# Performance work log

Measured on AMD Instinct MI355X. Metric: run time of the kernel, lower is better.

The kernel has to match this reference:

```python
import jax, jax.numpy as jnp
import numpy as np

B, NB, DIM = 4096, 64, 256
CNT_R = 500
CNT_E = CNT_R * 2  # padding relation id == CNT_E maps to the masked row
N_WR = CNT_R * 2 + 1
N_ZQ = CNT_R * 2


def setup_inputs() -> dict:
    key = jax.random.key(0)
    ks = jax.random.split(key, 10)
    batch_nei_rid = jax.random.randint(ks[0], (B, NB), 0, N_WR, dtype=jnp.int64 if jax.config.read('jax_enable_x64') else jnp.int32)
    batch_nei_e_emb = jax.random.normal(ks[1], (B, NB, DIM), dtype=jnp.float32)
    batch_nei_rw = jax.random.uniform(ks[2], (B, NB), dtype=jnp.float32)
    batch_q_rid = jax.random.randint(ks[3], (B,), 0, N_ZQ, dtype=jnp.int32)
    # xavier-normal-ish params
    def xav(k, shape):
        fan_in, fan_out = shape[-1], shape[-2] if len(shape) > 1 else shape[-1]
        std = (2.0 / (fan_in + fan_out)) ** 0.5
        return (jax.random.normal(k, shape) * std).astype(jnp.float32)
    w_r_weight = xav(ks[4], (N_WR, DIM))
    zq_weight = xav(ks[5], (N_ZQ, DIM))
    attn_W_w = xav(ks[6], (2 * DIM, 2 * DIM))   # [out, in], torch Linear layout
    attn_W_b = jnp.zeros((2 * DIM,), jnp.float32)
    u_a_w = xav(ks[7], (1, 2 * DIM))
    u_a_b = jnp.zeros((1,), jnp.float32)
    return {
        'batch_nei_rid': batch_nei_rid,
        'batch_nei_e_emb': batch_nei_e_emb,
        'batch_nei_rw': batch_nei_rw,
        'batch_q_rid': batch_q_rid,
        'w_r_weight': w_r_weight,
        'zq_weight': zq_weight,
        'attn_W_w': attn_W_w,
        'attn_W_b': attn_W_b,
        'u_a_w': u_a_w,
        'u_a_b': u_a_b,
    }


def reference(batch_nei_rid, batch_nei_e_emb, batch_nei_rw, batch_q_rid,
              w_r_weight, zq_weight, attn_W_w, attn_W_b, u_a_w, u_a_b):
    # relation hyperplane gather + TransH-style projection
    w_r = w_r_weight[batch_nei_rid]                                   # [B,NB,D]
    nrm = jnp.maximum(jnp.linalg.norm(w_r, axis=-1, keepdims=True), 1e-12)
    wn = w_r / nrm                                                    # f.normalize(p=2)
    e_tr = batch_nei_e_emb - jnp.sum(batch_nei_e_emb * wn, axis=-1, keepdims=True) * wn
    # mask_emb: 1 for real rows, 0 for padding row (index CNT_E)
    mask = (batch_nei_rid < CNT_E).astype(e_tr.dtype)[..., None]
    e_tr = e_tr * mask
    # nn attention: concat(z_q, e_Tr) -> Linear -> tanh -> Linear(1)
    z_q = zq_weight[batch_q_rid][:, None, :]                          # [B,1,D]
    cat = jnp.concatenate([jnp.broadcast_to(z_q, e_tr.shape), e_tr], axis=-1)  # [B,NB,2D]
    h = jnp.tanh(jnp.einsum('bni,oi->bno', cat, attn_W_w) + attn_W_b)
    _alpha = jnp.einsum('bni,oi->bno', h, u_a_w)[..., 0] + u_a_b[0]   # [B,NB]
    # mask_weight: 1e19 at padding row, subtracted before softmax
    _alpha = _alpha - jnp.where(batch_nei_rid == CNT_E, jnp.asarray(1e19, _alpha.dtype), jnp.asarray(0.0, _alpha.dtype))
    alpha = jax.nn.softmax(_alpha, axis=-1)
    attn = alpha + batch_nei_rw                                       # use_logic_attention
    return jnp.sum(attn[..., None] * e_tr, axis=-2)                   # [B,D]
```

## Files before the change

### kernel.cpp

```cpp
#include <hip/hip_runtime.h>
#include <math.h>

#define NB    64
#define DIM   256
#define TWOD  512
#define CNTE  1000
#define E2S   264

typedef __attribute__((ext_vector_type(8))) short short8;
typedef __attribute__((ext_vector_type(4))) float f32x4;

union U16x8 { uint4 u; short8 s; };

__device__ __forceinline__ unsigned short f2bf(float x) {
    unsigned int u = __float_as_uint(x);
    u += 0x7fffu + ((u >> 16) & 1u);
    return (unsigned short)(u >> 16);
}
__device__ __forceinline__ float bf2f(unsigned short h) {
    return __uint_as_float(((unsigned int)h) << 16);
}
__device__ __forceinline__ float tanh_fast(float x) {
    float e = __expf(2.0f * x);
    return 1.0f - 2.0f / (e + 1.0f);
}

__global__ __launch_bounds__(256) void pack_w_kernel(
    const float* __restrict__ attn_W, unsigned short* __restrict__ wbf)
{
    int f = blockIdx.x * 256 + threadIdx.x;
    int j    = f & 7;
    int lane = (f >> 3) & 63;
    int kt   = (f >> 9) & 15;
    int ot   = f >> 13;
    int o = ot * 16 + (lane & 15);
    int k = kt * 32 + (lane >> 4) * 8 + j;
    wbf[f] = f2bf(attn_W[(size_t)o * TWOD + k]);
}

__global__ __launch_bounds__(256, 2) void encoder_attn_kernel(
    const int*   __restrict__ nei_rid,
    const float* __restrict__ nei_e,
    const float* __restrict__ nei_rw,
    const int*   __restrict__ q_rid,
    const float* __restrict__ w_r,
    const float* __restrict__ zq_w,
    const float* __restrict__ attn_b,
    const float* __restrict__ u_a_w,
    const float* __restrict__ u_a_b,
    const unsigned short* __restrict__ wbf,
    float*       __restrict__ out)
{
    __shared__ __align__(16) unsigned short e2[NB * E2S];
    __shared__ __align__(16) unsigned short zq2[DIM];
    __shared__ float2 bua[TWOD];
    __shared__ float  red_a[256];
    __shared__ float  pen[NB];
    __shared__ float  attn_lds[NB];

    const int b = blockIdx.x;
    const int t = threadIdx.x;

    const int qr = q_rid[b];
    bua[t]       = make_float2(attn_b[t],       u_a_w[t]);
    bua[t + 256] = make_float2(attn_b[t + 256], u_a_w[t + 256]);
    zq2[t] = f2bf(zq_w[(size_t)qr * DIM + t]);

    const int n = t >> 2, q = t & 3;
    const int rid = nei_rid[b * NB + n];
    const float4* e4 = (const float4*)(nei_e + ((size_t)(b * NB + n)) * DIM) + q * 16;
    const float4* w4 = (const float4*)(w_r + (size_t)rid * DIM) + q * 16;
    {
        float4 ev[16], wv[16];
        float sew = 0.f, sww = 0.f;
        #pragma unroll
        for (int j = 0; j < 16; ++j) {
            ev[j] = e4[j]; wv[j] = w4[j];
            sew += ev[j].x * wv[j].x + ev[j].y * wv[j].y + ev[j].z * wv[j].z + ev[j].w * wv[j].w;
            sww += wv[j].x * wv[j].x + wv[j].y * wv[j].y + wv[j].z * wv[j].z + wv[j].w * wv[j].w;
        }
        sew += __shfl_xor(sew, 1); sew += __shfl_xor(sew, 2);
        sww += __shfl_xor(sww, 1); sww += __shfl_xor(sww, 2);
        float nc   = fmaxf(sqrtf(sww), 1e-12f);
        float coef = sew / (nc * nc);
        float maskf = (rid < CNTE) ? 1.f : 0.f;
        if (q == 0) pen[n] = (rid == CNTE) ? 1e19f : 0.f;
        unsigned short* e2row = e2 + n * E2S + q * 64;
        #pragma unroll
        for (int jj = 0; jj < 8; ++jj) {
            float4 e0 = ev[jj * 2],     w0 = wv[jj * 2];
            float4 e1 = ev[jj * 2 + 1], w1 = wv[jj * 2 + 1];
            uint4 pk;
            pk.x = (unsigned int)f2bf((e0.x - coef * w0.x) * maskf)
                 | ((unsigned int)f2bf((e0.y - coef * w0.y) * maskf) << 16);
            pk.y = (unsigned int)f2bf((e0.z - coef * w0.z) * maskf)
                 | ((unsigned int)f2bf((e0.w - coef * w0.w) * maskf) << 16);
            pk.z = (unsigned int)f2bf((e1.x - coef * w1.x) * maskf)
                 | ((unsigned int)f2bf((e1.y - coef * w1.y) * maskf) << 16);
            pk.w = (unsigned int)f2bf((e1.z - coef * w1.z) * maskf)
                 | ((unsigned int)f2bf((e1.w - coef * w1.w) * maskf) << 16);
            *(uint4*)(e2row + jj * 8) = pk;
        }
    }
    __syncthreads();

    const int wv_id = t >> 6;
    const int lane  = t & 63;
    const int l15 = lane & 15, lq = lane >> 4;

    short8 afrag[4][8];
    #pragma unroll
    for (int mt = 0; mt < 4; ++mt)
        #pragma unroll
        for (int kt = 0; kt < 8; ++kt) {
            const unsigned short* p = e2 + (mt * 16 + l15) * E2S + kt * 32 + lq * 8;
            U16x8 u; u.u = *(const uint4*)p;
            afrag[mt][kt] = u.s;
        }

    f32x4 lpv[4];
    #pragma unroll
    for (int mt = 0; mt < 4; ++mt) lpv[mt] = (f32x4){0.f, 0.f, 0.f, 0.f};

    #pragma unroll 1
    for (int ot = 0; ot < 8; ++ot) {
        const int otg = wv_id * 8 + ot;
        const uint4* wp = (const uint4*)wbf + (size_t)(otg * 16) * 64 + lane;
        short8 bz[8], be[8];
        #pragma unroll
        for (int kt = 0; kt < 8; ++kt) { U16x8 u; u.u = wp[kt * 64]; bz[kt] = u.s; }
        #pragma unroll
        for (int kt = 0; kt < 8; ++kt) { U16x8 u; u.u = wp[(kt + 8) * 64]; be[kt] = u.s; }

        f32x4 accz = (f32x4){0.f, 0.f, 0.f, 0.f};
        #pragma unroll
        for (int kt = 0; kt < 8; ++kt) {
            U16x8 u; u.u = *(const uint4*)(zq2 + kt * 32 + lq * 8);
            accz = __builtin_amdgcn_mfma_f32_16x16x32_bf16(u.s, bz[kt], accz, 0, 0, 0);
        }
        f32x4 acc[4];
        #pragma unroll
        for (int mt = 0; mt < 4; ++mt) acc[mt] = accz;
        #pragma unroll
        for (int kt = 0; kt < 8; ++kt)
            #pragma unroll
            for (int mt = 0; mt < 4; ++mt)
                acc[mt] = __builtin_amdgcn_mfma_f32_16x16x32_bf16(
                              afrag[mt][kt], be[kt], acc[mt], 0, 0, 0);

        float2 zu = bua[otg * 16 + l15];
        #pragma unroll
        for (int mt = 0; mt < 4; ++mt)
            #pragma unroll
            for (int r = 0; r < 4; ++r) {
                float h = tanh_fast(acc[mt][r] + zu.x);
                lpv[mt][r] += zu.y * h;
            }
    }

    #pragma unroll
    for (int mt = 0; mt < 4; ++mt)
        #pragma unroll
        for (int r = 0; r < 4; ++r) {
            float v = lpv[mt][r];
            v += __shfl_xor(v, 1); v += __shfl_xor(v, 2);
            v += __shfl_xor(v, 4); v += __shfl_xor(v, 8);
            if (l15 == 0) red_a[wv_id * 64 + mt * 16 + lq * 4 + r] = v;
        }
    __syncthreads();

    if (t < NB) {
        float lgt = red_a[t] + red_a[64 + t] + red_a[128 + t] + red_a[192 + t]
                  + u_a_b[0] - pen[t];
        float m = lgt;
        #pragma unroll
        for (int off = 32; off > 0; off >>= 1) m = fmaxf(m, __shfl_xor(m, off));
        float ex = __expf(lgt - m);
        float s = ex;
        #pragma unroll
        for (int off = 32; off > 0; off >>= 1) s += __shfl_xor(s, off);
        attn_lds[t] = ex / s + nei_rw[b * NB + t];
    }
    __syncthreads();

    float oacc = 0.f;
    #pragma unroll 8
    for (int nn = 0; nn < NB; ++nn)
        oacc += attn_lds[nn] * bf2f(e2[nn * E2S + t]);
    out[(size_t)b * DIM + t] = oacc;
}

extern "C" void kernel_launch(void* const* d_in, const int* in_sizes, int n_in,
                              void* d_out, int out_size, void* d_ws, size_t ws_size,
                              hipStream_t stream) {
    const int*   nei_rid = (const int*)  d_in[0];
    const float* nei_e   = (const float*)d_in[1];
    const float* nei_rw  = (const float*)d_in[2];
    const int*   q_rid   = (const int*)  d_in[3];
    const float* w_r     = (const float*)d_in[4];
    const float* zq_w    = (const float*)d_in[5];
    const float* attn_W  = (const float*)d_in[6];
    const float* attn_b  = (const float*)d_in[7];
    const float* u_a_w   = (const float*)d_in[8];
    const float* u_a_b   = (const float*)d_in[9];
    float* out = (float*)d_out;

    const int B = in_sizes[3];

    unsigned short* wbf = (unsigned short*)d_ws;

    hipLaunchKernelGGL(pack_w_kernel, dim3(1024), dim3(256), 0, stream, attn_W, wbf);
    hipLaunchKernelGGL(encoder_attn_kernel, dim3(B), dim3(256), 0, stream,
                       nei_rid, nei_e, nei_rw, q_rid, w_r, zq_w,
                       attn_b, u_a_w, u_a_b, wbf, out);
}
```

Measured before the change: 526.4 us.

## Precompute z_q projection per query id and restructure MFMA loop over k

Splits the attention linear layer: the z_q half is precomputed once per query relation id (1000 ids) in a separate fp32 kernel and gathered per batch row, so only the e_tr half (K=256) runs as bf16 MFMA. A fallback computes the z_q projection inside the block when workspace is too small. The MFMA loop is reordered to hold all 8 output tiles of accumulators and stream A fragments per k-step, and tanh is folded algebraically into a reciprocal, dropping the constant u_a_b and bias terms that cancel in softmax. The neighbour projection is reworked so 8 threads handle each row over two halves. Holding more accumulators raises register pressure, and the extra launch adds a small fixed cost.

```diff
diff --git a/kernel.cpp b/kernel.cpp
--- a/kernel.cpp
+++ b/kernel.cpp
@@ -6,6 +6,7 @@
 #define TWOD  512
 #define CNTE  1000
 #define E2S   264
+#define NQ    1000
 
 typedef __attribute__((ext_vector_type(8))) short short8;
 typedef __attribute__((ext_vector_type(4))) float f32x4;
@@ -20,9 +21,37 @@
 __device__ __forceinline__ float bf2f(unsigned short h) {
     return __uint_as_float(((unsigned int)h) << 16);
 }
-__device__ __forceinline__ float tanh_fast(float x) {
-    float e = __expf(2.0f * x);
-    return 1.0f - 2.0f / (e + 1.0f);
+
+__global__ __launch_bounds__(256) void zpre_kernel(
+    const float* __restrict__ zq_w, const float* __restrict__ attn_W,
+    const float* __restrict__ attn_b, float* __restrict__ zpre)
+{
+    __shared__ float zq[8][DIM];
+    const int t  = threadIdx.x;
+    const int q0 = blockIdx.x * 8;
+    #pragma unroll
+    for (int r = 0; r < 8; ++r) zq[r][t] = zq_w[(size_t)(q0 + r) * DIM + t];
+    __syncthreads();
+    #pragma unroll
+    for (int half = 0; half < 2; ++half) {
+        const int o = t + half * 256;
+        const float4* wrow = (const float4*)(attn_W + (size_t)o * TWOD);
+        float acc[8];
+        #pragma unroll
+        for (int r = 0; r < 8; ++r) acc[r] = 0.f;
+        #pragma unroll 4
+        for (int kk = 0; kk < 64; ++kk) {
+            float4 w = wrow[kk];
+            #pragma unroll
+            for (int r = 0; r < 8; ++r)
+                acc[r] += w.x * zq[r][kk * 4 + 0] + w.y * zq[r][kk * 4 + 1]
+                        + w.z * zq[r][kk * 4 + 2] + w.w * zq[r][kk * 4 + 3];
+        }
+        const float bo = attn_b[o];
+        #pragma unroll
+        for (int r = 0; r < 8; ++r)
+            zpre[(size_t)(q0 + r) * TWOD + o] = acc[r] + bo;
+    }
 }
 
 __global__ __launch_bounds__(256) void pack_w_kernel(
@@ -31,11 +60,11 @@
     int f = blockIdx.x * 256 + threadIdx.x;
     int j    = f & 7;
     int lane = (f >> 3) & 63;
-    int kt   = (f >> 9) & 15;
-    int ot   = f >> 13;
-    int o = ot * 16 + (lane & 15);
-    int k = kt * 32 + (lane >> 4) * 8 + j;
-    wbf[f] = f2bf(attn_W[(size_t)o * TWOD + k]);
+    int kt   = (f >> 9) & 7;
+    int ot   = f >> 12;
+    int o  = ot * 16 + (lane & 15);
+    int ke = kt * 32 + (lane >> 4) * 8 + j;
+    wbf[f] = f2bf(attn_W[(size_t)o * TWOD + 256 + ke]);
 }
 
 __global__ __launch_bounds__(256, 2) void encoder_attn_kernel(
@@ -45,61 +74,83 @@
     const int*   __restrict__ q_rid,
     const float* __restrict__ w_r,
     const float* __restrict__ zq_w,
+    const float* __restrict__ attn_W,
     const float* __restrict__ attn_b,
     const float* __restrict__ u_a_w,
-    const float* __restrict__ u_a_b,
+    const float* __restrict__ zpre,
     const unsigned short* __restrict__ wbf,
-    float*       __restrict__ out)
+    float*       __restrict__ out,
+    int has_zpre)
 {
     __shared__ __align__(16) unsigned short e2[NB * E2S];
-    __shared__ __align__(16) unsigned short zq2[DIM];
-    __shared__ float2 bua[TWOD];
-    __shared__ float  red_a[256];
+    __shared__ float2 zu[TWOD];
+    __shared__ __align__(16) float red_a[256];
     __shared__ float  pen[NB];
     __shared__ float  attn_lds[NB];
 
     const int b = blockIdx.x;
     const int t = threadIdx.x;
-
     const int qr = q_rid[b];
-    bua[t]       = make_float2(attn_b[t],       u_a_w[t]);
-    bua[t + 256] = make_float2(attn_b[t + 256], u_a_w[t + 256]);
-    zq2[t] = f2bf(zq_w[(size_t)qr * DIM + t]);
-
-    const int n = t >> 2, q = t & 3;
-    const int rid = nei_rid[b * NB + n];
-    const float4* e4 = (const float4*)(nei_e + ((size_t)(b * NB + n)) * DIM) + q * 16;
-    const float4* w4 = (const float4*)(w_r + (size_t)rid * DIM) + q * 16;
+
+    if (has_zpre) {
+        zu[t]       = make_float2(zpre[(size_t)qr * TWOD + t],       u_a_w[t]);
+        zu[t + 256] = make_float2(zpre[(size_t)qr * TWOD + t + 256], u_a_w[t + 256]);
+    } else {
+        red_a[t] = zq_w[(size_t)qr * DIM + t];
+        __syncthreads();
+        float a0 = 0.f, a1 = 0.f;
+        const float4* w0 = (const float4*)(attn_W + (size_t)t * TWOD);
+        const float4* w1 = (const float4*)(attn_W + (size_t)(t + 256) * TWOD);
+        const float4* zz = (const float4*)red_a;
+        #pragma unroll 8
+        for (int kk = 0; kk < 64; ++kk) {
+            float4 z = zz[kk], u0 = w0[kk], u1 = w1[kk];
+            a0 += u0.x * z.x + u0.y * z.y + u0.z * z.z + u0.w * z.w;
+            a1 += u1.x * z.x + u1.y * z.y + u1.z * z.z + u1.w * z.w;
+        }
+        zu[t]       = make_float2(a0 + attn_b[t],       u_a_w[t]);
+        zu[t + 256] = make_float2(a1 + attn_b[t + 256], u_a_w[t + 256]);
+        __syncthreads();
+    }
+
     {
-        float4 ev[16], wv[16];
-        float sew = 0.f, sww = 0.f;
-        #pragma unroll
-        for (int j = 0; j < 16; ++j) {
-            ev[j] = e4[j]; wv[j] = w4[j];
-            sew += ev[j].x * wv[j].x + ev[j].y * wv[j].y + ev[j].z * wv[j].z + ev[j].w * wv[j].w;
-            sww += wv[j].x * wv[j].x + wv[j].y * wv[j].y + wv[j].z * wv[j].z + wv[j].w * wv[j].w;
-        }
-        sew += __shfl_xor(sew, 1); sew += __shfl_xor(sew, 2);
-        sww += __shfl_xor(sww, 1); sww += __shfl_xor(sww, 2);
-        float nc   = fmaxf(sqrtf(sww), 1e-12f);
-        float coef = sew / (nc * nc);
-        float maskf = (rid < CNTE) ? 1.f : 0.f;
-        if (q == 0) pen[n] = (rid == CNTE) ? 1e19f : 0.f;
-        unsigned short* e2row = e2 + n * E2S + q * 64;
-        #pragma unroll
-        for (int jj = 0; jj < 8; ++jj) {
-            float4 e0 = ev[jj * 2],     w0 = wv[jj * 2];
-            float4 e1 = ev[jj * 2 + 1], w1 = wv[jj * 2 + 1];
-            uint4 pk;
-            pk.x = (unsigned int)f2bf((e0.x - coef * w0.x) * maskf)
-                 | ((unsigned int)f2bf((e0.y - coef * w0.y) * maskf) << 16);
-            pk.y = (unsigned int)f2bf((e0.z - coef * w0.z) * maskf)
-                 | ((unsigned int)f2bf((e0.w - coef * w0.w) * maskf) << 16);
-            pk.z = (unsigned int)f2bf((e1.x - coef * w1.x) * maskf)
-                 | ((unsigned int)f2bf((e1.y - coef * w1.y) * maskf) << 16);
-            pk.w = (unsigned int)f2bf((e1.z - coef * w1.z) * maskf)
-                 | ((unsigned int)f2bf((e1.w - coef * w1.w) * maskf) << 16);
-            *(uint4*)(e2row + jj * 8) = pk;
+        const int q = t & 7;
+        #pragma unroll
+        for (int half = 0; half < 2; ++half) {
+            const int n = (t >> 3) + half * 32;
+            const int rid = nei_rid[b * NB + n];
+            const float4* e4 = (const float4*)(nei_e + ((size_t)(b * NB + n)) * DIM) + q * 8;
+            const float4* w4 = (const float4*)(w_r + (size_t)rid * DIM) + q * 8;
+            float4 ev[8], wv[8];
+            float sew = 0.f, sww = 0.f;
+            #pragma unroll
+            for (int j = 0; j < 8; ++j) {
+                ev[j] = e4[j]; wv[j] = w4[j];
+                sew += ev[j].x * wv[j].x + ev[j].y * wv[j].y + ev[j].z * wv[j].z + ev[j].w * wv[j].w;
+                sww += wv[j].x * wv[j].x + wv[j].y * wv[j].y + wv[j].z * wv[j].z + wv[j].w * wv[j].w;
+            }
+            sew += __shfl_xor(sew, 1); sew += __shfl_xor(sew, 2); sew += __shfl_xor(sew, 4);
+            sww += __shfl_xor(sww, 1); sww += __shfl_xor(sww, 2); sww += __shfl_xor(sww, 4);
+            float nc   = fmaxf(sqrtf(sww), 1e-12f);
+            float coef = sew / (nc * nc);
+            float maskf = (rid < CNTE) ? 1.f : 0.f;
+            if (q == 0) pen[n] = (rid == CNTE) ? 1e19f : 0.f;
+            unsigned short* e2row = e2 + n * E2S + q * 32;
+            #pragma unroll
+            for (int jj = 0; jj < 4; ++jj) {
+                float4 e0 = ev[jj * 2],     w0 = wv[jj * 2];
+                float4 e1 = ev[jj * 2 + 1], w1 = wv[jj * 2 + 1];
+                uint4 pk;
+                pk.x = (unsigned int)f2bf((e0.x - coef * w0.x) * maskf)
+                     | ((unsigned int)f2bf((e0.y - coef * w0.y) * maskf) << 16);
+                pk.y = (unsigned int)f2bf((e0.z - coef * w0.z) * maskf)
+                     | ((unsigned int)f2bf((e0.w - coef * w0.w) * maskf) << 16);
+                pk.z = (unsigned int)f2bf((e1.x - coef * w1.x) * maskf)
+                     | ((unsigned int)f2bf((e1.y - coef * w1.y) * maskf) << 16);
+                pk.w = (unsigned int)f2bf((e1.z - coef * w1.z) * maskf)
+                     | ((unsigned int)f2bf((e1.w - coef * w1.w) * maskf) << 16);
+                *(uint4*)(e2row + jj * 8) = pk;
+            }
         }
     }
     __syncthreads();
@@ -108,53 +159,46 @@
     const int lane  = t & 63;
     const int l15 = lane & 15, lq = lane >> 4;
 
-    short8 afrag[4][8];
-    #pragma unroll
-    for (int mt = 0; mt < 4; ++mt)
-        #pragma unroll
-        for (int kt = 0; kt < 8; ++kt) {
-            const unsigned short* p = e2 + (mt * 16 + l15) * E2S + kt * 32 + lq * 8;
-            U16x8 u; u.u = *(const uint4*)p;
-            afrag[mt][kt] = u.s;
-        }
+    f32x4 acc[8][4];
+    #pragma unroll
+    for (int oo = 0; oo < 8; ++oo) {
+        const float zx = zu[(wv_id * 8 + oo) * 16 + l15].x;
+        #pragma unroll
+        for (int mt = 0; mt < 4; ++mt) acc[oo][mt] = (f32x4){zx, zx, zx, zx};
+    }
+
+    #pragma unroll
+    for (int kt = 0; kt < 8; ++kt) {
+        short8 afr[4];
+        #pragma unroll
+        for (int mt = 0; mt < 4; ++mt) {
+            U16x8 u; u.u = *(const uint4*)(e2 + (mt * 16 + l15) * E2S + kt * 32 + lq * 8);
+            afr[mt] = u.s;
+        }
+        #pragma unroll
+        for (int oo = 0; oo < 8; ++oo) {
+            U16x8 u;
+            u.u = ((const uint4*)wbf)[(size_t)((wv_id * 8 + oo) * 8 + kt) * 64 + lane];
+            #pragma unroll
+            for (int mt = 0; mt < 4; ++mt)
+                acc[oo][mt] = __builtin_amdgcn_mfma_f32_16x16x32_bf16(
+                                  afr[mt], u.s, acc[oo][mt], 0, 0, 0);
+        }
+    }
 
     f32x4 lpv[4];
     #pragma unroll
     for (int mt = 0; mt < 4; ++mt) lpv[mt] = (f32x4){0.f, 0.f, 0.f, 0.f};
-
-    #pragma unroll 1
-    for (int ot = 0; ot < 8; ++ot) {
-        const int otg = wv_id * 8 + ot;
-        const uint4* wp = (const uint4*)wbf + (size_t)(otg * 16) * 64 + lane;
-        short8 bz[8], be[8];
-        #pragma unroll
-        for (int kt = 0; kt < 8; ++kt) { U16x8 u; u.u = wp[kt * 64]; bz[kt] = u.s; }
-        #pragma unroll
-        for (int kt = 0; kt < 8; ++kt) { U16x8 u; u.u = wp[(kt + 8) * 64]; be[kt] = u.s; }
-
-        f32x4 accz = (f32x4){0.f, 0.f, 0.f, 0.f};
-        #pragma unroll
-        for (int kt = 0; kt < 8; ++kt) {
-            U16x8 u; u.u = *(const uint4*)(zq2 + kt * 32 + lq * 8);
-            accz = __builtin_amdgcn_mfma_f32_16x16x32_bf16(u.s, bz[kt], accz, 0, 0, 0);
-        }
-        f32x4 acc[4];
-        #pragma unroll
-        for (int mt = 0; mt < 4; ++mt) acc[mt] = accz;
-        #pragma unroll
-        for (int kt = 0; kt < 8; ++kt)
-            #pragma unroll
-            for (int mt = 0; mt < 4; ++mt)
-                acc[mt] = __builtin_amdgcn_mfma_f32_16x16x32_bf16(
-                              afrag[mt][kt], be[kt], acc[mt], 0, 0, 0);
-
-        float2 zu = bua[otg * 16 + l15];
+    #pragma unroll
+    for (int oo = 0; oo < 8; ++oo) {
+        const float uy2 = -2.0f * zu[(wv_id * 8 + oo) * 16 + l15].y;
         #pragma unroll
         for (int mt = 0; mt < 4; ++mt)
             #pragma unroll
             for (int r = 0; r < 4; ++r) {
-                float h = tanh_fast(acc[mt][r] + zu.x);
-                lpv[mt][r] += zu.y * h;
+                float x = acc[oo][mt][r];
+                float e = __expf(x + x);
+                lpv[mt][r] += uy2 * __builtin_amdgcn_rcpf(e + 1.0f);
             }
     }
 
@@ -171,7 +215,7 @@
 
     if (t < NB) {
         float lgt = red_a[t] + red_a[64 + t] + red_a[128 + t] + red_a[192 + t]
-                  + u_a_b[0] - pen[t];
+                  - pen[t];
         float m = lgt;
         #pragma unroll
         for (int off = 32; off > 0; off >>= 1) m = fmaxf(m, __shfl_xor(m, off));
@@ -202,15 +246,24 @@
     const float* attn_W  = (const float*)d_in[6];
     const float* attn_b  = (const float*)d_in[7];
     const float* u_a_w   = (const float*)d_in[8];
-    const float* u_a_b   = (const float*)d_in[9];
+
     float* out = (float*)d_out;
-
     const int B = in_sizes[3];
 
-    unsigned short* wbf = (unsigned short*)d_ws;
-
-    hipLaunchKernelGGL(pack_w_kernel, dim3(1024), dim3(256), 0, stream, attn_W, wbf);
+    const size_t ZPRE_BYTES = (size_t)NQ * TWOD * 4;
+    const size_t WBF_BYTES  = (size_t)512 * 256 * 2;
+    const int has_zpre = (ws_size >= ZPRE_BYTES + WBF_BYTES) ? 1 : 0;
+
+    float*          zpre = (float*)d_ws;
+    unsigned short* wbf  = has_zpre
+        ? (unsigned short*)((char*)d_ws + ZPRE_BYTES)
+        : (unsigned short*)d_ws;
+
+    if (has_zpre)
+        hipLaunchKernelGGL(zpre_kernel, dim3(NQ / 8), dim3(256), 0, stream,
+                           zq_w, attn_W, attn_b, zpre);
+    hipLaunchKernelGGL(pack_w_kernel, dim3(512), dim3(256), 0, stream, attn_W, wbf);
     hipLaunchKernelGGL(encoder_attn_kernel, dim3(B), dim3(256), 0, stream,
-                       nei_rid, nei_e, nei_rw, q_rid, w_r, zq_w,
-                       attn_b, u_a_w, u_a_b, wbf, out);
-}
+                       nei_rid, nei_e, nei_rw, q_rid, w_r, zq_w, attn_W, attn_b,
+                       u_a_w, zpre, wbf, out, has_zpre);
+}
```

Measured after the change: 586.1 us. 11.3% more time.
